# Kernel tuning notes

Hardware: AMD Instinct MI355X
Metric: run time of the kernel (lower is better)

## Reference

```python
import jax, jax.numpy as jnp
import numpy as np

HEADS = 8
FEATURE = 512
COMPUTE = 256
SEQ = 512
BATCH = 64


def setup_inputs() -> dict:
    key = jax.random.key(0)
    ks = jax.random.split(key, 10)
    d1 = jax.random.normal(ks[0], (BATCH, FEATURE), dtype=jnp.float32)
    d2 = jax.random.normal(ks[1], (SEQ, BATCH, FEATURE), dtype=jnp.float32)
    # linear1: Linear(FEATURE -> COMPUTE) + ReLU
    w1 = jax.random.normal(ks[2], (FEATURE, COMPUTE), dtype=jnp.float32) * (1.0 / np.sqrt(FEATURE))
    b1 = jnp.zeros((COMPUTE,), dtype=jnp.float32)
    # per-head score params, stacked: ws[i] is [2C, C], ps[i] is [C, 1]
    W = jax.random.normal(ks[3], (HEADS, 2 * COMPUTE, COMPUTE), dtype=jnp.float32)
    P = jax.random.normal(ks[4], (HEADS, COMPUTE), dtype=jnp.float32)
    # value projection weight_v: [FEATURE, COMPUTE]
    wv = jax.random.normal(ks[5], (FEATURE, COMPUTE), dtype=jnp.float32)
    # cc: Linear(COMPUTE*HEADS -> 128) + ReLU
    wcc = jax.random.normal(ks[6], (COMPUTE * HEADS, 128), dtype=jnp.float32) * (1.0 / np.sqrt(COMPUTE * HEADS))
    bcc = jnp.zeros((128,), dtype=jnp.float32)
    return {"d1": d1, "d2": d2, "w1": w1, "b1": b1, "W": W, "P": P,
            "wv": wv, "wcc": wcc, "bcc": bcc, "d2_size": SEQ}


def reference(d1, d2, w1, b1, W, P, wv, wcc, bcc, d2_size):
    S, B, F = d2.shape
    # linear1 on flattened d2 rows -> [S*B, C]
    d3 = jax.nn.relu(d2.reshape(-1, F) @ w1 + b1)
    # linear1 on d1, tiled S times along batch axis -> [S*B, C]
    d4 = jax.nn.relu(d1 @ w1 + b1)            # [B, C]
    d4 = jnp.tile(d4, (S, 1))                  # [S*B, C]
    d5 = jnp.concatenate([d3, d4], axis=1).reshape(S, B, -1)  # [S, B, 2C]
    # value path: tanh(d2 @ weight_v) -> [B, S, C]
    tv = jnp.tanh(jnp.einsum('sbf,fc->sbc', d2, wv)).transpose(1, 0, 2)
    # all heads batched: us = tanh(d5 @ W_h) -> [H, S, B, C]
    us = jnp.tanh(jnp.einsum('sbd,hdc->hsbc', d5, W))
    atts = jnp.einsum('hsbc,hc->hbs', us, P)   # [H, B, S]
    scores = jax.nn.softmax(atts, axis=-1)     # softmax over sequence
    vs = jnp.einsum('hbs,bsc->hbc', scores, tv)  # weighted sum over S -> [H, B, C]
    # torch.cat(vs, dim=1): head-major concat -> [B, H*C]
    vs = vs.transpose(1, 0, 2).reshape(B, -1)
    return jax.nn.relu(vs @ wcc + bcc)         # [B, 128]
```

## Files before the change

kernel.cpp:

```cpp
#include <hip/hip_runtime.h>
#include <cstddef>
#include <cstdint>

#define HH 8
#define FF 512
#define CC 256
#define SS 512
#define BB 64
#define SB (SS*BB)

typedef __attribute__((ext_vector_type(4))) float f32x4;
typedef __attribute__((ext_vector_type(8))) short bf16x8;

typedef __attribute__((address_space(1))) unsigned int gu32_t;
typedef __attribute__((address_space(3))) unsigned int lu32_t;

__device__ __forceinline__ void gld16(const void* gp, void* lp) {
    __builtin_amdgcn_global_load_lds((gu32_t*)gp, (lu32_t*)lp, 16, 0, 0);
}

__device__ __forceinline__ float fast_tanh(float x) {
    float e = __expf(2.0f * x);
    return 1.0f - 2.0f / (e + 1.0f);
}
__device__ __forceinline__ float relu_f(float x) { return fmaxf(x, 0.0f); }

__device__ __forceinline__ unsigned short f2bf(float x) {
    unsigned u = __float_as_uint(x);
    unsigned r = u + 0x7FFFu + ((u >> 16) & 1u);
    return (unsigned short)(r >> 16);
}
__device__ __forceinline__ float bf2f(unsigned short h) {
    return __uint_as_float(((unsigned)h) << 16);
}


__global__ __launch_bounds__(256) void p_prep(
    const float* __restrict__ w1, const float* __restrict__ wv,
    const float* __restrict__ W, const float* __restrict__ d1,
    const float* __restrict__ b1,
    unsigned short* __restrict__ w1ts, unsigned short* __restrict__ wvts,
    unsigned short* __restrict__ Wts, float* __restrict__ d4)
{
    __shared__ float T[64][65];
    __shared__ float As[16][68];
    __shared__ float Bs[16][68];
    const int tid = threadIdx.x;
    const int bid = blockIdx.x;
    if (bid < 192) {
        const float* src;
        unsigned short* dst;
        int kt64, nt;
        if (bid < 64) {
            int m = bid >> 5;
            int t = bid & 31;
            kt64 = t >> 2; nt = t & 3;
            src = m ? wv : w1;
            dst = m ? wvts : w1ts;
        } else {
            int t = bid - 64;
            int h = t >> 4; int tt = t & 15;
            kt64 = tt >> 2; nt = tt & 3;
            src = W + (size_t)h * 2 * CC * CC;
            dst = Wts + (size_t)h * 8 * CC * 64;
        }
        const int k0 = kt64 * 64, n0 = nt * 64;
        #pragma unroll
        for (int jj = 0; jj < 4; ++jj) {
            int i = (tid >> 4) + jj * 16;
            int j = (tid & 15) * 4;
            float4 v = *(const float4*)(src + (size_t)(k0 + i) * CC + n0 + j);
            T[i][j] = v.x; T[i][j+1] = v.y; T[i][j+2] = v.z; T[i][j+3] = v.w;
        }
        __syncthreads();
        {
            const int n_local = tid & 63;
            const int kg = (tid >> 6) * 16;
            const int n_abs = n0 + n_local;
            const int sxn = n_abs & 7;
            #pragma unroll
            for (int j = 0; j < 2; ++j) {
                const int kbase = kg + j * 8;
                const int k_abs = k0 + kbase;
                const int kt = k_abs >> 5;
                const int g = (k_abs >> 3) & 3;
                bf16x8 hv8, lv8;
                #pragma unroll
                for (int q = 0; q < 8; ++q) {
                    float x = T[kbase + q][n_local];
                    unsigned short hx = f2bf(x);
                    hv8[q] = (short)hx;
                    lv8[q] = (short)f2bf(x - bf2f(hx));
                }
                size_t rowo = ((size_t)kt * CC + n_abs) * 64;
                *(bf16x8*)(dst + rowo + (size_t)((2*g + 0) ^ sxn) * 8) = hv8;
                *(bf16x8*)(dst + rowo + (size_t)((2*g + 1) ^ sxn) * 8) = lv8;
            }
        }
    } else {
        const int n0 = (bid - 192) * 64;
        const int tx = tid & 15, ty = tid >> 4;
        const int lm = tid >> 2, lk4 = (tid & 3) * 4;
        const int bk = tid >> 4, bn4 = (tid & 15) * 4;
        float acc[4][4] = {};
        for (int k0 = 0; k0 < FF; k0 += 16) {
            float4 a = *(const float4*)(d1 + (size_t)lm * FF + k0 + lk4);
            As[lk4+0][lm] = a.x; As[lk4+1][lm] = a.y;
            As[lk4+2][lm] = a.z; As[lk4+3][lm] = a.w;
            *(float4*)&Bs[bk][bn4] = *(const float4*)(w1 + (size_t)(k0+bk)*CC + n0 + bn4);
            __syncthreads();
            #pragma unroll
            for (int kk = 0; kk < 16; ++kk) {
                float4 a4 = *(const float4*)&As[kk][ty*4];
                float4 b4 = *(const float4*)&Bs[kk][tx*4];
                float av[4] = {a4.x, a4.y, a4.z, a4.w};
                float bv[4] = {b4.x, b4.y, b4.z, b4.w};
                #pragma unroll
                for (int i = 0; i < 4; ++i)
                    #pragma unroll
                    for (int j = 0; j < 4; ++j)
                        acc[i][j] = fmaf(av[i], bv[j], acc[i][j]);
            }
            __syncthreads();
        }
        #pragma unroll
        for (int i = 0; i < 4; ++i) {
            int row = ty*4 + i;
            #pragma unroll
            for (int j = 0; j < 4; ++j)
                d4[(size_t)row*CC + n0 + tx*4 + j] = relu_f(acc[i][j] + b1[n0 + tx*4 + j]);
        }
    }
}

__global__ __launch_bounds__(256, 2) void k1_main(
    const float* __restrict__ d2,
    const unsigned short* __restrict__ w1ts, const unsigned short* __restrict__ wvts,
    const float* __restrict__ b1,
    const float* __restrict__ d4, const float* __restrict__ W,
    unsigned short* __restrict__ d3s, unsigned short* __restrict__ tv,
    float* __restrict__ e4)
{
    __shared__ __align__(16) unsigned short Abuf[128 * 64];
    __shared__ __align__(16) unsigned short Bbuf[256 * 64];

    const int tid = threadIdx.x;
    const int bid = blockIdx.x;

    if (bid >= 512) {
        float (*As)[68] = (float(*)[68])&Abuf[0];
        float (*Bs)[68] = (float(*)[68])&Bbuf[0];
        const int idx = bid - 512;
        const int n0 = (idx & 3) * 64;
        const int h  = idx >> 2;
        const float* Wh = W + ((size_t)h * 2 * CC + CC) * CC;
        const int tx = tid & 15, ty = tid >> 4;
        const int lm = tid >> 2, lk4 = (tid & 3) * 4;
        const int bk = tid >> 4, bn4 = (tid & 15) * 4;
        float acc[4][4] = {};
        for (int k0 = 0; k0 < CC; k0 += 16) {
            float4 a = *(const float4*)(d4 + (size_t)lm * CC + k0 + lk4);
            As[lk4+0][lm] = a.x; As[lk4+1][lm] = a.y;
            As[lk4+2][lm] = a.z; As[lk4+3][lm] = a.w;
            *(float4*)&Bs[bk][bn4] = *(const float4*)(Wh + (size_t)(k0+bk)*CC + n0 + bn4);
            __syncthreads();
            #pragma unroll
            for (int kk = 0; kk < 16; ++kk) {
                float4 a4 = *(const float4*)&As[kk][ty*4];
                float4 b4 = *(const float4*)&Bs[kk][tx*4];
                float av[4] = {a4.x, a4.y, a4.z, a4.w};
                float bv[4] = {b4.x, b4.y, b4.z, b4.w};
                #pragma unroll
                for (int i = 0; i < 4; ++i)
                    #pragma unroll
                    for (int j = 0; j < 4; ++j)
                        acc[i][j] = fmaf(av[i], bv[j], acc[i][j]);
            }
            __syncthreads();
        }
        #pragma unroll
        for (int i = 0; i < 4; ++i) {
            int b = ty*4 + i;
            #pragma unroll
            for (int j = 0; j < 4; ++j)
                e4[((size_t)h*BB + b)*CC + n0 + tx*4 + j] = acc[i][j];
        }
        return;
    }

    const int path = bid >> 8;
    const int r0 = (bid & 255) * 128;
    const int lane = tid & 63, w = tid >> 6;
    const int rowgrp = w & 1, colgrp = w >> 1;
    const int cb = lane & 15, quad = lane >> 4;
    const unsigned short* BT = path ? wvts : w1ts;

    f32x4 acc[4][8];
    f32x4 zero = {0.0f, 0.0f, 0.0f, 0.0f};
    #pragma unroll
    for (int rt = 0; rt < 4; ++rt)
        #pragma unroll
        for (int ct = 0; ct < 8; ++ct) acc[rt][ct] = zero;

    const int ar = tid >> 1, ak = (tid & 1) * 16;
    const int arx = ar & 7;
    const int g0 = ak >> 3;
    const int phi = (2 * quad) ^ (cb & 7);

    for (int k0 = 0; k0 < FF; k0 += 32) {
        const int kt = k0 >> 5;
        {
            const unsigned short* Bsrc = BT + (size_t)kt * (CC * 64);
            #pragma unroll
            for (int i = 0; i < 8; ++i) {
                int chunk = i * 4 + w;
                gld16(Bsrc + (size_t)chunk * 512 + lane * 8, &Bbuf[chunk * 512]);
            }
        }
        {
            const float* s = d2 + (size_t)(r0 + ar) * FF + k0 + ak;
            float v[16];
            *(float4*)&v[0]  = *(const float4*)(s);
            *(float4*)&v[4]  = *(const float4*)(s + 4);
            *(float4*)&v[8]  = *(const float4*)(s + 8);
            *(float4*)&v[12] = *(const float4*)(s + 12);
            bf16x8 vh0, vh1, vl0, vl1;
            #pragma unroll
            for (int j = 0; j < 8; ++j) {
                unsigned short h = f2bf(v[j]);
                vh0[j] = (short)h; vl0[j] = (short)f2bf(v[j] - bf2f(h));
                unsigned short h2 = f2bf(v[j+8]);
                vh1[j] = (short)h2; vl1[j] = (short)f2bf(v[j+8] - bf2f(h2));
            }
            unsigned short* Ar = &Abuf[ar * 64];
            *(bf16x8*)&Ar[((2*g0 + 0) ^ arx) * 8] = vh0;
            *(bf16x8*)&Ar[((2*g0 + 1) ^ arx) * 8] = vl0;
            *(bf16x8*)&Ar[((2*g0 + 2) ^ arx) * 8] = vh1;
            *(bf16x8*)&Ar[((2*g0 + 3) ^ arx) * 8] = vl1;
        }
        __syncthreads();
        bf16x8 ahf[4], alf[4];
        #pragma unroll
        for (int rt = 0; rt < 4; ++rt) {
            const unsigned short* Arow = &Abuf[(rowgrp*64 + rt*16 + cb) * 64];
            ahf[rt] = *(const bf16x8*)&Arow[phi * 8];
            alf[rt] = *(const bf16x8*)&Arow[(phi ^ 1) * 8];
        }
        #pragma unroll
        for (int ct = 0; ct < 8; ++ct) {
            const unsigned short* Brow = &Bbuf[(colgrp*128 + ct*16 + cb) * 64];
            bf16x8 bh = *(const bf16x8*)&Brow[phi * 8];
            bf16x8 bl = *(const bf16x8*)&Brow[(phi ^ 1) * 8];
            #pragma unroll
            for (int rt = 0; rt < 4; ++rt) {
                acc[rt][ct] = __builtin_amdgcn_mfma_f32_16x16x32_bf16(ahf[rt], bh, acc[rt][ct], 0, 0, 0);
                acc[rt][ct] = __builtin_amdgcn_mfma_f32_16x16x32_bf16(ahf[rt], bl, acc[rt][ct], 0, 0, 0);
                acc[rt][ct] = __builtin_amdgcn_mfma_f32_16x16x32_bf16(alf[rt], bh, acc[rt][ct], 0, 0, 0);
            }
        }
        __syncthreads();
    }
    if (path == 0) {
        float bias[8];
        #pragma unroll
        for (int ct = 0; ct < 8; ++ct) bias[ct] = b1[colgrp*128 + ct*16 + cb];
        #pragma unroll
        for (int rt = 0; rt < 4; ++rt) {
            #pragma unroll
            for (int r = 0; r < 4; ++r) {
                int gr = r0 + rowgrp*64 + rt*16 + quad*4 + r;
                int sxr = gr & 7;
                #pragma unroll
                for (int ct = 0; ct < 8; ++ct) {
                    int c = colgrp*128 + ct*16 + cb;
                    float val = relu_f(acc[rt][ct][r] + bias[ct]);
                    unsigned short hx = f2bf(val);
                    unsigned short lx = f2bf(val - bf2f(hx));
                    int kt = c >> 5;
                    int g = (c >> 3) & 3;
                    size_t rowo = ((size_t)kt * SB + gr) * 64;
                    d3s[rowo + (size_t)((2*g + 0) ^ sxr) * 8 + (c & 7)] = hx;
                    d3s[rowo + (size_t)((2*g + 1) ^ sxr) * 8 + (c & 7)] = lx;
                }
            }
        }
    } else {
        #pragma unroll
        for (int rt = 0; rt < 4; ++rt) {
            #pragma unroll
            for (int r = 0; r < 4; ++r) {
                int gr = r0 + rowgrp*64 + rt*16 + quad*4 + r;
                int s = gr >> 6, b = gr & 63;
                #pragma unroll
                for (int ct = 0; ct < 8; ++ct) {
                    int c = colgrp*128 + ct*16 + cb;
                    tv[((size_t)b * SS + s) * CC + c] = f2bf(fast_tanh(acc[rt][ct][r]));
                }
            }
        }
    }
}

__global__ __launch_bounds__(512, 2) void k3_atts(
    const unsigned short* __restrict__ d3s, const unsigned short* __restrict__ Wts,
    const float* __restrict__ e4, const float* __restrict__ P,
    float* __restrict__ atts)
{
    __shared__ __align__(16) unsigned short Abuf[2][256 * 64];
    __shared__ __align__(16) unsigned short Bbuf[2][256 * 64];
    __shared__ float red[2][256];

    const int tid = threadIdx.x;
    const int lane = tid & 63, w = tid >> 6;
    const int h = blockIdx.y;
    const int r0 = blockIdx.x * 256;
    const int rowgrp = w & 3, colgrp = w >> 2;
    const int cb = lane & 15, quad = lane >> 4;
    const int phi = (2 * quad) ^ (cb & 7);

    const unsigned short* Wh = Wts + (size_t)h * (8 * CC * 64);

    f32x4 acc[4][8];
    f32x4 zero = {0.0f, 0.0f, 0.0f, 0.0f};
    #pragma unroll
    for (int rt = 0; rt < 4; ++rt)
        #pragma unroll
        for (int ct = 0; ct < 8; ++ct) acc[rt][ct] = zero;

    auto STAGE = [&](int buf, int kt) {
        const unsigned short* Asrc = d3s + ((size_t)kt * SB + r0) * 64;
        const unsigned short* Bsrc = Wh + (size_t)kt * (CC * 64);
        #pragma unroll
        for (int i = 0; i < 4; ++i) {
            int chunk = i * 8 + w;
            gld16(Asrc + (size_t)chunk * 512 + lane * 8, &Abuf[buf][chunk * 512]);
        }
        #pragma unroll
        for (int i = 0; i < 4; ++i) {
            int chunk = i * 8 + w;
            gld16(Bsrc + (size_t)chunk * 512 + lane * 8, &Bbuf[buf][chunk * 512]);
        }
    };

    auto COMPUTE = [&](int buf) {
        bf16x8 ahf[4], alf[4];
        #pragma unroll
        for (int rt = 0; rt < 4; ++rt) {
            const unsigned short* Arow = &Abuf[buf][(rowgrp*64 + rt*16 + cb) * 64];
            ahf[rt] = *(const bf16x8*)&Arow[phi * 8];
            alf[rt] = *(const bf16x8*)&Arow[(phi ^ 1) * 8];
        }
        __builtin_amdgcn_s_setprio(1);
        #pragma unroll
        for (int ct = 0; ct < 8; ++ct) {
            const unsigned short* Brow = &Bbuf[buf][(colgrp*128 + ct*16 + cb) * 64];
            bf16x8 bh = *(const bf16x8*)&Brow[phi * 8];
            bf16x8 bl = *(const bf16x8*)&Brow[(phi ^ 1) * 8];
            #pragma unroll
            for (int rt = 0; rt < 4; ++rt) {
                acc[rt][ct] = __builtin_amdgcn_mfma_f32_16x16x32_bf16(ahf[rt], bh, acc[rt][ct], 0, 0, 0);
                acc[rt][ct] = __builtin_amdgcn_mfma_f32_16x16x32_bf16(ahf[rt], bl, acc[rt][ct], 0, 0, 0);
                acc[rt][ct] = __builtin_amdgcn_mfma_f32_16x16x32_bf16(alf[rt], bh, acc[rt][ct], 0, 0, 0);
            }
        }
        __builtin_amdgcn_s_setprio(0);
    };

    STAGE(0, 0);
    asm volatile("s_waitcnt vmcnt(0)" ::: "memory");
    __builtin_amdgcn_s_barrier();
    __builtin_amdgcn_sched_barrier(0);

    #pragma unroll
    for (int kt = 0; kt < 8; ++kt) {
        if (kt < 7) STAGE((kt + 1) & 1, kt + 1);
        COMPUTE(kt & 1);
        if (kt < 7) {
            asm volatile("s_waitcnt vmcnt(0)" ::: "memory");
            __builtin_amdgcn_s_barrier();
            __builtin_amdgcn_sched_barrier(0);
        }
    }

    float Pv[8];
    #pragma unroll
    for (int ct = 0; ct < 8; ++ct) Pv[ct] = P[(size_t)h * CC + colgrp*128 + ct*16 + cb];
    #pragma unroll
    for (int rt = 0; rt < 4; ++rt) {
        #pragma unroll
        for (int r = 0; r < 4; ++r) {
            int b = rt*16 + quad*4 + r;
            const float* e4p = e4 + ((size_t)h * BB + b) * CC + colgrp*128 + cb;
            float part = 0.0f;
            #pragma unroll
            for (int ct = 0; ct < 8; ++ct) {
                float u = acc[rt][ct][r] + e4p[ct*16];
                part = fmaf(Pv[ct], fast_tanh(u), part);
            }
            part += __shfl_xor(part, 1); part += __shfl_xor(part, 2);
            part += __shfl_xor(part, 4); part += __shfl_xor(part, 8);
            if (cb == 0) red[colgrp][rowgrp*64 + b] = part;
        }
    }
    __syncthreads();
    if (tid < 256) {
        float v = red[0][tid] + red[1][tid];
        int gr = r0 + tid;
        int s = gr >> 6, b = gr & 63;
        atts[((size_t)h * BB + b) * SS + s] = v;
    }
}

__global__ __launch_bounds__(256) void k456_out(
    const float* __restrict__ atts, const unsigned short* __restrict__ tv,
    const float* __restrict__ wcc, const float* __restrict__ bcc,
    float* __restrict__ out)
{
    __shared__ float sc[HH][SS];
    __shared__ float red[4][2048];
    const int b = blockIdx.x;
    const int tid = threadIdx.x;
    const int lane = tid & 63, w = tid >> 6;

    for (int i = tid; i < HH*SS; i += 256) {
        int h = i >> 9, s = i & 511;
        sc[h][s] = atts[((size_t)h*BB + b)*SS + s];
    }
    __syncthreads();
    #pragma unroll
    for (int t = 0; t < 2; ++t) {
        int hh = w*2 + t;
        float x[8];
        #pragma unroll
        for (int j = 0; j < 8; ++j) x[j] = sc[hh][j*64 + lane];
        float m = x[0];
        #pragma unroll
        for (int j = 1; j < 8; ++j) m = fmaxf(m, x[j]);
        #pragma unroll
        for (int d = 1; d < 64; d <<= 1) m = fmaxf(m, __shfl_xor(m, d));
        float sum = 0.0f;
        #pragma unroll
        for (int j = 0; j < 8; ++j) { x[j] = __expf(x[j] - m); sum += x[j]; }
        #pragma unroll
        for (int d = 1; d < 64; d <<= 1) sum += __shfl_xor(sum, d);
        float inv = 1.0f / sum;
        #pragma unroll
        for (int j = 0; j < 8; ++j) sc[hh][j*64 + lane] = x[j] * inv;
    }
    __syncthreads();
    {
        const int cl = tid & 63, stripe = tid >> 6;
        const int c0 = cl * 4;
        const unsigned short* tvb = tv + ((size_t)b * SS + stripe * 128) * CC + c0;
        float acc[HH][4] = {};
        for (int si = 0; si < 128; ++si) {
            uint2 u = *(const uint2*)(tvb + (size_t)si * CC);
            float x0 = bf2f((unsigned short)(u.x));
            float x1 = bf2f((unsigned short)(u.x >> 16));
            float x2 = bf2f((unsigned short)(u.y));
            float x3 = bf2f((unsigned short)(u.y >> 16));
            int s = stripe * 128 + si;
            #pragma unroll
            for (int h = 0; h < HH; ++h) {
                float wgt = sc[h][s];
                acc[h][0] = fmaf(wgt, x0, acc[h][0]);
                acc[h][1] = fmaf(wgt, x1, acc[h][1]);
                acc[h][2] = fmaf(wgt, x2, acc[h][2]);
                acc[h][3] = fmaf(wgt, x3, acc[h][3]);
            }
        }
        #pragma unroll
        for (int h = 0; h < HH; ++h)
            #pragma unroll
            for (int j = 0; j < 4; ++j)
                red[stripe][h*256 + c0 + j] = acc[h][j];
    }
    __syncthreads();
    for (int i = tid; i < 2048; i += 256)
        red[0][i] = red[0][i] + red[1][i] + red[2][i] + red[3][i];
    __syncthreads();
    {
        const int n = tid & 127, half = tid >> 7;
        float o = 0.0f;
        const int kbase = half * 1024;
        for (int k = 0; k < 1024; ++k)
            o = fmaf(red[0][kbase + k], wcc[(size_t)(kbase + k) * 128 + n], o);
        float* r2 = &sc[0][0];
        r2[half * 128 + n] = o;
    }
    __syncthreads();
    if (tid < 128)
        out[(size_t)b * 128 + tid] = relu_f(sc[0][tid] + sc[0][128 + tid] + bcc[tid]);
}

extern "C" void kernel_launch(void* const* d_in, const int* in_sizes, int n_in,
                              void* d_out, int out_size, void* d_ws, size_t ws_size,
                              hipStream_t stream)
{
    (void)in_sizes; (void)n_in; (void)out_size; (void)ws_size;
    const float* d1  = (const float*)d_in[0];
    const float* d2  = (const float*)d_in[1];
    const float* w1  = (const float*)d_in[2];
    const float* b1  = (const float*)d_in[3];
    const float* W   = (const float*)d_in[4];
    const float* P   = (const float*)d_in[5];
    const float* wv  = (const float*)d_in[6];
    const float* wcc = (const float*)d_in[7];
    const float* bcc = (const float*)d_in[8];
    float* out = (float*)d_out;

    char* p = (char*)d_ws;
    unsigned short* d3s  = (unsigned short*)p; p += (size_t)8 * SB * 64 * 2;
    unsigned short* tv   = (unsigned short*)p; p += (size_t)SB * CC * 2;
    unsigned short* w1ts = (unsigned short*)p; p += (size_t)16 * CC * 64 * 2;
    unsigned short* wvts = (unsigned short*)p; p += (size_t)16 * CC * 64 * 2;
    unsigned short* Wts  = (unsigned short*)p; p += (size_t)HH * 8 * CC * 64 * 2;
    float* d4   = (float*)p;  p += (size_t)BB * CC * 4;
    float* e4   = (float*)p;  p += (size_t)HH * BB * CC * 4;
    float* atts = (float*)p;  p += (size_t)HH * BB * SS * 4;

    p_prep   <<<dim3(196),       256, 0, stream>>>(w1, wv, W, d1, b1,
                  w1ts, wvts, Wts, d4);
    k1_main  <<<dim3(544),       256, 0, stream>>>(d2, w1ts, wvts, b1, d4, W,
                  d3s, tv, e4);
    k3_atts  <<<dim3(128, HH),   512, 0, stream>>>(d3s, Wts, e4, P, atts);
    k456_out <<<dim3(BB),        256, 0, stream>>>(atts, tv, wcc, bcc, out);
}
```

Baseline: 367.9 us.

## Keep d3 tile resident in registers and loop over all heads per block

k3_atts now launches one block per sequence position (64 rows), loads its A tile once into LDS and then registers, and iterates over all 8 heads, streaming each head's W slices through a double buffer. This removes the eightfold re-read of d3s across heads in exchange for smaller per-block tiles (64x256 per head), a large register-held A fragment array that may reduce occupancy, and per-head epilogue syncs.

```diff
diff --git a/kernel.cpp b/kernel.cpp
--- a/kernel.cpp
+++ b/kernel.cpp
@@ -301,113 +301,146 @@
     }
 }
 
-__global__ __launch_bounds__(512, 2) void k3_atts(
+__global__ __launch_bounds__(512) void k3_atts(
     const unsigned short* __restrict__ d3s, const unsigned short* __restrict__ Wts,
     const float* __restrict__ e4, const float* __restrict__ P,
     float* __restrict__ atts)
 {
-    __shared__ __align__(16) unsigned short Abuf[2][256 * 64];
+    __shared__ __align__(16) unsigned short Abuf[8 * 64 * 64];
     __shared__ __align__(16) unsigned short Bbuf[2][256 * 64];
-    __shared__ float red[2][256];
+    __shared__ float red[4][64];
 
     const int tid = threadIdx.x;
     const int lane = tid & 63, w = tid >> 6;
-    const int h = blockIdx.y;
-    const int r0 = blockIdx.x * 256;
-    const int rowgrp = w & 3, colgrp = w >> 2;
+    const int r0 = blockIdx.x * 64;
+    const int s_idx = blockIdx.x;
+    const int rowgrp = w & 1, colgrp = w >> 1;
     const int cb = lane & 15, quad = lane >> 4;
     const int phi = (2 * quad) ^ (cb & 7);
 
-    const unsigned short* Wh = Wts + (size_t)h * (8 * CC * 64);
-
-    f32x4 acc[4][8];
-    f32x4 zero = {0.0f, 0.0f, 0.0f, 0.0f};
     #pragma unroll
-    for (int rt = 0; rt < 4; ++rt)
-        #pragma unroll
-        for (int ct = 0; ct < 8; ++ct) acc[rt][ct] = zero;
-
-    auto STAGE = [&](int buf, int kt) {
-        const unsigned short* Asrc = d3s + ((size_t)kt * SB + r0) * 64;
-        const unsigned short* Bsrc = Wh + (size_t)kt * (CC * 64);
+    for (int i = 0; i < 8; ++i) {
+        int chunk = i * 8 + w;
+        int kt = chunk >> 3, sub = chunk & 7;
+        gld16(d3s + ((size_t)kt * SB + r0 + sub * 8) * 64 + (size_t)lane * 8,
+              &Abuf[chunk * 512]);
+    }
+    {
         #pragma unroll
         for (int i = 0; i < 4; ++i) {
             int chunk = i * 8 + w;
-            gld16(Asrc + (size_t)chunk * 512 + lane * 8, &Abuf[buf][chunk * 512]);
-        }
-        #pragma unroll
-        for (int i = 0; i < 4; ++i) {
-            int chunk = i * 8 + w;
-            gld16(Bsrc + (size_t)chunk * 512 + lane * 8, &Bbuf[buf][chunk * 512]);
-        }
-    };
-
-    auto COMPUTE = [&](int buf) {
-        bf16x8 ahf[4], alf[4];
-        #pragma unroll
-        for (int rt = 0; rt < 4; ++rt) {
-            const unsigned short* Arow = &Abuf[buf][(rowgrp*64 + rt*16 + cb) * 64];
-            ahf[rt] = *(const bf16x8*)&Arow[phi * 8];
-            alf[rt] = *(const bf16x8*)&Arow[(phi ^ 1) * 8];
-        }
-        __builtin_amdgcn_s_setprio(1);
-        #pragma unroll
-        for (int ct = 0; ct < 8; ++ct) {
-            const unsigned short* Brow = &Bbuf[buf][(colgrp*128 + ct*16 + cb) * 64];
-            bf16x8 bh = *(const bf16x8*)&Brow[phi * 8];
-            bf16x8 bl = *(const bf16x8*)&Brow[(phi ^ 1) * 8];
-            #pragma unroll
-            for (int rt = 0; rt < 4; ++rt) {
-                acc[rt][ct] = __builtin_amdgcn_mfma_f32_16x16x32_bf16(ahf[rt], bh, acc[rt][ct], 0, 0, 0);
-                acc[rt][ct] = __builtin_amdgcn_mfma_f32_16x16x32_bf16(ahf[rt], bl, acc[rt][ct], 0, 0, 0);
-                acc[rt][ct] = __builtin_amdgcn_mfma_f32_16x16x32_bf16(alf[rt], bh, acc[rt][ct], 0, 0, 0);
-            }
-        }
-        __builtin_amdgcn_s_setprio(0);
-    };
-
-    STAGE(0, 0);
+            gld16(Wts + (size_t)chunk * 512 + (size_t)lane * 8, &Bbuf[0][chunk * 512]);
+        }
+    }
     asm volatile("s_waitcnt vmcnt(0)" ::: "memory");
     __builtin_amdgcn_s_barrier();
     __builtin_amdgcn_sched_barrier(0);
 
+    auto STAGEB = [&](int buf, int h, int kt) {
+        const unsigned short* Bsrc = Wts + ((size_t)h * 8 + kt) * (CC * 64);
+        #pragma unroll
+        for (int i = 0; i < 4; ++i) {
+            int chunk = i * 8 + w;
+            gld16(Bsrc + (size_t)chunk * 512 + (size_t)lane * 8, &Bbuf[buf][chunk * 512]);
+        }
+    };
+
+    bf16x8 Areg[8][2][2];
+    f32x4 acc[2][4];
+    f32x4 zero = {0.0f, 0.0f, 0.0f, 0.0f};
+
+    auto EPILOGUE = [&](int h) {
+        float Pv[4];
+        #pragma unroll
+        for (int ct = 0; ct < 4; ++ct) Pv[ct] = P[(size_t)h * CC + colgrp*64 + ct*16 + cb];
+        #pragma unroll
+        for (int rt = 0; rt < 2; ++rt) {
+            #pragma unroll
+            for (int r = 0; r < 4; ++r) {
+                int b = rowgrp*32 + rt*16 + quad*4 + r;
+                const float* e4p = e4 + ((size_t)h * BB + b) * CC + colgrp*64 + cb;
+                float part = 0.0f;
+                #pragma unroll
+                for (int ct = 0; ct < 4; ++ct) {
+                    float u = acc[rt][ct][r] + e4p[ct*16];
+                    part = fmaf(Pv[ct], fast_tanh(u), part);
+                }
+                part += __shfl_xor(part, 1); part += __shfl_xor(part, 2);
+                part += __shfl_xor(part, 4); part += __shfl_xor(part, 8);
+                if (cb == 0) red[colgrp][b] = part;
+            }
+        }
+        __syncthreads();
+        if (tid < 64) {
+            float v = red[0][tid] + red[1][tid] + red[2][tid] + red[3][tid];
+            atts[((size_t)h * BB + tid) * SS + s_idx] = v;
+        }
+        __syncthreads();
+    };
+
+    #pragma unroll
+    for (int rt = 0; rt < 2; ++rt)
+        #pragma unroll
+        for (int ct = 0; ct < 4; ++ct) acc[rt][ct] = zero;
+
     #pragma unroll
     for (int kt = 0; kt < 8; ++kt) {
-        if (kt < 7) STAGE((kt + 1) & 1, kt + 1);
-        COMPUTE(kt & 1);
-        if (kt < 7) {
+        STAGEB((kt & 1) ^ 1, (kt == 7) ? 1 : 0, (kt + 1) & 7);
+        #pragma unroll
+        for (int rt = 0; rt < 2; ++rt) {
+            const unsigned short* Arow = &Abuf[kt * 4096 + (rowgrp*32 + rt*16 + cb) * 64];
+            Areg[kt][rt][0] = *(const bf16x8*)&Arow[phi * 8];
+            Areg[kt][rt][1] = *(const bf16x8*)&Arow[(phi ^ 1) * 8];
+        }
+        __builtin_amdgcn_s_setprio(1);
+        #pragma unroll
+        for (int ct = 0; ct < 4; ++ct) {
+            const unsigned short* Brow = &Bbuf[kt & 1][(colgrp*64 + ct*16 + cb) * 64];
+            bf16x8 bh = *(const bf16x8*)&Brow[phi * 8];
+            bf16x8 bl = *(const bf16x8*)&Brow[(phi ^ 1) * 8];
+            #pragma unroll
+            for (int rt = 0; rt < 2; ++rt) {
+                acc[rt][ct] = __builtin_amdgcn_mfma_f32_16x16x32_bf16(Areg[kt][rt][0], bh, acc[rt][ct], 0, 0, 0);
+                acc[rt][ct] = __builtin_amdgcn_mfma_f32_16x16x32_bf16(Areg[kt][rt][0], bl, acc[rt][ct], 0, 0, 0);
+                acc[rt][ct] = __builtin_amdgcn_mfma_f32_16x16x32_bf16(Areg[kt][rt][1], bh, acc[rt][ct], 0, 0, 0);
+            }
+        }
+        __builtin_amdgcn_s_setprio(0);
+        asm volatile("s_waitcnt vmcnt(0)" ::: "memory");
+        __builtin_amdgcn_s_barrier();
+        __builtin_amdgcn_sched_barrier(0);
+    }
+    EPILOGUE(0);
+
+    for (int h = 1; h < HH; ++h) {
+        #pragma unroll
+        for (int rt = 0; rt < 2; ++rt)
+            #pragma unroll
+            for (int ct = 0; ct < 4; ++ct) acc[rt][ct] = zero;
+
+        #pragma unroll
+        for (int kt = 0; kt < 8; ++kt) {
+            if (h < 7 || kt < 7)
+                STAGEB((kt & 1) ^ 1, (kt == 7) ? h + 1 : h, (kt + 1) & 7);
+            __builtin_amdgcn_s_setprio(1);
+            #pragma unroll
+            for (int ct = 0; ct < 4; ++ct) {
+                const unsigned short* Brow = &Bbuf[kt & 1][(colgrp*64 + ct*16 + cb) * 64];
+                bf16x8 bh = *(const bf16x8*)&Brow[phi * 8];
+                bf16x8 bl = *(const bf16x8*)&Brow[(phi ^ 1) * 8];
+                #pragma unroll
+                for (int rt = 0; rt < 2; ++rt) {
+                    acc[rt][ct] = __builtin_amdgcn_mfma_f32_16x16x32_bf16(Areg[kt][rt][0], bh, acc[rt][ct], 0, 0, 0);
+                    acc[rt][ct] = __builtin_amdgcn_mfma_f32_16x16x32_bf16(Areg[kt][rt][0], bl, acc[rt][ct], 0, 0, 0);
+                    acc[rt][ct] = __builtin_amdgcn_mfma_f32_16x16x32_bf16(Areg[kt][rt][1], bh, acc[rt][ct], 0, 0, 0);
+                }
+            }
+            __builtin_amdgcn_s_setprio(0);
             asm volatile("s_waitcnt vmcnt(0)" ::: "memory");
             __builtin_amdgcn_s_barrier();
             __builtin_amdgcn_sched_barrier(0);
         }
-    }
-
-    float Pv[8];
-    #pragma unroll
-    for (int ct = 0; ct < 8; ++ct) Pv[ct] = P[(size_t)h * CC + colgrp*128 + ct*16 + cb];
-    #pragma unroll
-    for (int rt = 0; rt < 4; ++rt) {
-        #pragma unroll
-        for (int r = 0; r < 4; ++r) {
-            int b = rt*16 + quad*4 + r;
-            const float* e4p = e4 + ((size_t)h * BB + b) * CC + colgrp*128 + cb;
-            float part = 0.0f;
-            #pragma unroll
-            for (int ct = 0; ct < 8; ++ct) {
-                float u = acc[rt][ct][r] + e4p[ct*16];
-                part = fmaf(Pv[ct], fast_tanh(u), part);
-            }
-            part += __shfl_xor(part, 1); part += __shfl_xor(part, 2);
-            part += __shfl_xor(part, 4); part += __shfl_xor(part, 8);
-            if (cb == 0) red[colgrp][rowgrp*64 + b] = part;
-        }
-    }
-    __syncthreads();
-    if (tid < 256) {
-        float v = red[0][tid] + red[1][tid];
-        int gr = r0 + tid;
-        int s = gr >> 6, b = gr & 63;
-        atts[((size_t)h * BB + b) * SS + s] = v;
+        EPILOGUE(h);
     }
 }
 
@@ -523,6 +556,6 @@
                   w1ts, wvts, Wts, d4);
     k1_main  <<<dim3(544),       256, 0, stream>>>(d2, w1ts, wvts, b1, d4, W,
                   d3s, tv, e4);
-    k3_atts  <<<dim3(128, HH),   512, 0, stream>>>(d3s, Wts, e4, P, atts);
+    k3_atts  <<<dim3(512),       512, 0, stream>>>(d3s, Wts, e4, P, atts);
     k456_out <<<dim3(BB),        256, 0, stream>>>(atts, tv, wcc, bcc, out);
 }
```

Result: slower. 437.7 us (+19.0%).
